# Performance work log

Hardware: AMD Instinct MI355X
Metric: run time of the kernel (lower is better)

## Reference

```python
import jax, jax.numpy as jnp
import numpy as np

B = 131072      # batch size
ORDER = 8       # number of TT modes
N = 64          # grid points per mode (dims[i])
R = 32          # internal TT rank
EPS = 1e-8      # stability_eps
INIT_SCALE = 0.01


def setup_inputs() -> dict:
    key = jax.random.key(0)
    k_idx, k0, kmid, klast = jax.random.split(key, 4)
    indices = jax.random.randint(k_idx, (B, ORDER), 0, N, dtype=jnp.int64)
    # TT cores: core0 (1, N, R), middle cores (ORDER-2, R, N, R), core_last (R, N, 1)
    core0 = jax.random.normal(k0, (1, N, R), dtype=jnp.float32) * INIT_SCALE
    cores_mid = jax.random.normal(kmid, (ORDER - 2, R, N, R), dtype=jnp.float32) * INIT_SCALE
    core_last = jax.random.normal(klast, (R, N, 1), dtype=jnp.float32) * INIT_SCALE
    return {"indices": indices, "core0": core0, "cores_mid": cores_mid, "core_last": core_last}


def _tt_forward(indices, core0, cores_mid, core_last):
    order = 2 + cores_mid.shape[0]
    dims = jnp.array([core0.shape[1]] + [cores_mid.shape[2]] * cores_mid.shape[0]
                     + [core_last.shape[1]], dtype=indices.dtype)
    idx = jnp.clip(indices, 0, dims[None, :] - 1)

    # i == 0: core0[:, idx, :] -> [1, B, R] -> squeeze leading rank-1 -> [B, R]
    v = core0[0, idx[:, 0], :]

    def step(v, core, col_idx):
        sl = core[:, col_idx, :]                                  # [R, B, R']
        norm = jnp.linalg.norm(v, axis=1, keepdims=True) + EPS    # [B, 1]
        v_new = jnp.einsum('br,rbs->bs', v / norm, sl) * norm     # [B, R']
        return v_new

    # middle cores share shape -> scan over them (gather + normalized matvec chain)
    def scan_body(v, inputs):
        core, col = inputs
        return step(v, core, col), None

    mid_cols = idx[:, 1:order - 1].T  # [ORDER-2, B]
    v, _ = jax.lax.scan(scan_body, v, (cores_mid, mid_cols))

    # last core -> [B, 1] -> squeeze -> [B]
    v = step(v, core_last, idx[:, order - 1])
    return v[:, 0]


def reference(indices, core0, cores_mid, core_last):
    return _tt_forward(indices, core0, cores_mid, core_last)
```

## Files before the change

kernel.cpp:

```cpp
#include <hip/hip_runtime.h>
#include <hip/hip_fp16.h>


#define B_TOTAL 131072
#define NDIM 64
#define RANK 32
#define S_BLK 512
#define THREADS 512
#define VSTRIDE_H 40

typedef _Float16 half8  __attribute__((ext_vector_type(8)));
typedef float    f32x4  __attribute__((ext_vector_type(4)));

__global__ __launch_bounds__(256) void build_tables(
    const float* __restrict__ core0, const float* __restrict__ mid,
    const float* __restrict__ lastc,
    half8* __restrict__ PKB, __half* __restrict__ T01, float* __restrict__ TL)
{
    const int id = blockIdx.x * 256 + threadIdx.x;
    if (id < 32768) {
        const int l  = id & 63;
        const int f  = (id >> 6) & 1;
        const int c  = (id >> 7) & 63;
        const int tt = id >> 13;
        const int q = l >> 4, li = l & 15;
        const int n = f * 16 + li;
        const int t = 1 + tt;
        half8 h;
        #pragma unroll
        for (int j = 0; j < 8; ++j) {
            const int k = q * 8 + j;
            h[j] = (_Float16)(16.0f * mid[((t * 32 + k) * 64 + c) * 32 + n]);
        }
        PKB[id] = h;
    } else if (id < 163840) {
        const int i2 = id - 32768;
        const int s = i2 & 31, c1 = (i2 >> 5) & 63, c0 = i2 >> 11;
        float acc = 0.f;
        #pragma unroll
        for (int r = 0; r < 32; ++r)
            acc = fmaf(core0[c0 * 32 + r], mid[(r * 64 + c1) * 32 + s], acc);
        T01[(c0 * 64 + c1) * 32 + s] = __float2half(acc * 256.0f);
    } else {
        const int i3 = id - 163840;
        const int c7 = i3 & 63, c6 = (i3 >> 6) & 63, r = i3 >> 12;
        const float* m5 = mid + 5 * 65536;
        float acc = 0.f;
        #pragma unroll
        for (int s = 0; s < 32; ++s)
            acc = fmaf(m5[(r * 64 + c6) * 32 + s], lastc[s * 64 + c7], acc);
        TL[(c6 * 64 + c7) * 32 + r] = acc * 256.0f;
    }
}

__global__ __launch_bounds__(512) void tt_main_mfma(
    const int* __restrict__ idx, const __half* __restrict__ T01,
    const half8* __restrict__ PKB, const float* __restrict__ TL,
    float* __restrict__ out)
{
    __shared__ __align__(16) __half vbuf[S_BLK * VSTRIDE_H];
    __shared__ unsigned short ord[4][S_BLK];
    __shared__ unsigned char  cols[S_BLK][8];
    __shared__ unsigned int   bases[4][65];
    __shared__ unsigned int   hist[64];

    const int tid  = threadIdx.x;
    const int lane = tid & 63;
    const int wv   = tid >> 6;
    const int li   = lane & 15;
    const int quad = lane >> 4;
    const int b0   = blockIdx.x * S_BLK;

    #pragma unroll
    for (int k = 0; k < S_BLK * 8; k += THREADS) {
        const int lin = k + tid;
        int v = idx[b0 * 8 + lin];
        v = min(max(v, 0), NDIM - 1);
        cols[lin >> 3][lin & 7] = (unsigned char)v;
    }
    __syncthreads();

    for (int tt = 0; tt < 4; ++tt) {
        if (tid < 64) hist[tid] = 0;
        __syncthreads();
        const unsigned int key = cols[tid][2 + tt];
        const unsigned int rank = atomicAdd(&hist[key], 1u);
        __syncthreads();
        if (tid < 64) {
            const unsigned int v = hist[tid];
            unsigned int inc = v;
            #pragma unroll
            for (int d = 1; d < 64; d <<= 1) {
                const unsigned int n = __shfl_up(inc, d);
                if (lane >= d) inc += n;
            }
            bases[tt][tid] = inc - v;
            if (tid == 63) bases[tt][64] = inc;
        }
        __syncthreads();
        ord[tt][bases[tt][key] + rank] = (unsigned short)tid;
        __syncthreads();
    }

    {
        const int g = tid & 7, gid = tid >> 3;
        #pragma unroll
        for (int it = 0; it < S_BLK / 64; ++it) {
            const int s = it * 64 + gid;
            const int c0 = cols[s][0], c1 = cols[s][1];
            const uint2 q = *reinterpret_cast<const uint2*>(
                T01 + (c0 * 64 + c1) * 32 + 4 * g);
            unsigned int* vp = reinterpret_cast<unsigned int*>(vbuf) + s * (VSTRIDE_H / 2);
            vp[2 * g]     = q.x;
            vp[2 * g + 1] = q.y;
        }
    }
    __syncthreads();

    for (int tt = 0; tt < 4; ++tt) {
        for (int c = wv * 8; c < wv * 8 + 8; ++c) {
            const int start = (int)bases[tt][c];
            const int end   = (int)bases[tt][c + 1];
            if (start == end) continue;
            const half8 bf0 = PKB[((tt * 64 + c) * 2 + 0) * 64 + lane];
            const half8 bf1 = PKB[((tt * 64 + c) * 2 + 1) * 64 + lane];

            for (int p = start; p < end; p += 16) {
                const int pos = min(p + li, end - 1);
                const int sm  = (int)ord[tt][pos];
                const half8 A = *reinterpret_cast<const half8*>(
                    reinterpret_cast<const char*>(vbuf) + sm * 80 + quad * 16);
                f32x4 d0 = {0.f, 0.f, 0.f, 0.f}, d1 = {0.f, 0.f, 0.f, 0.f};
                d0 = __builtin_amdgcn_mfma_f32_16x16x32_f16(A, bf0, d0, 0, 0, 0);
                d1 = __builtin_amdgcn_mfma_f32_16x16x32_f16(A, bf1, d1, 0, 0, 0);
                #pragma unroll
                for (int r = 0; r < 4; ++r) {
                    const int mrow = quad * 4 + r;
                    const int s2 = __shfl(sm, mrow);
                    if (p + mrow < end) {
                        vbuf[s2 * VSTRIDE_H + li]      = __float2half(d0[r]);
                        vbuf[s2 * VSTRIDE_H + 16 + li] = __float2half(d1[r]);
                    }
                }
            }
        }
        __syncthreads();
    }

    {
        const int g = tid & 7, gid = tid >> 3;
        #pragma unroll
        for (int it = 0; it < S_BLK / 64; ++it) {
            const int s = it * 64 + gid;
            const int c6 = cols[s][6], c7 = cols[s][7];
            const unsigned int* vp =
                reinterpret_cast<const unsigned int*>(vbuf) + s * (VSTRIDE_H / 2);
            const __half2 v01 = *reinterpret_cast<const __half2*>(&vp[2 * g]);
            const __half2 v23 = *reinterpret_cast<const __half2*>(&vp[2 * g + 1]);
            const float4 L = *reinterpret_cast<const float4*>(
                TL + (c6 * 64 + c7) * 32 + 4 * g);
            float o = 0.f;
            o = fmaf(__low2float(v01),  L.x, o);
            o = fmaf(__high2float(v01), L.y, o);
            o = fmaf(__low2float(v23),  L.z, o);
            o = fmaf(__high2float(v23), L.w, o);
            o += __shfl_xor(o, 1);
            o += __shfl_xor(o, 2);
            o += __shfl_xor(o, 4);
            if (g == 0) out[b0 + s] = o * 2.3283064365386963e-10f;
        }
    }
}

#define PKB_OFF 0u
#define TL_OFF  524288u
#define T01_OFF 1048576u

extern "C" void kernel_launch(void* const* d_in, const int* in_sizes, int n_in,
                              void* d_out, int out_size, void* d_ws, size_t ws_size,
                              hipStream_t stream) {
    const int*   idx   = (const int*)d_in[0];
    const float* core0 = (const float*)d_in[1];
    const float* mid   = (const float*)d_in[2];
    const float* lastc = (const float*)d_in[3];
    float* out = (float*)d_out;

    half8*  PKB = (half8*)((char*)d_ws + PKB_OFF);
    float*  TL  = (float*)((char*)d_ws + TL_OFF);
    __half* T01 = (__half*)((char*)d_ws + T01_OFF);

    hipLaunchKernelGGL(build_tables, dim3(294912 / 256), dim3(256), 0, stream,
                       core0, mid, lastc, PKB, T01, TL);
    hipLaunchKernelGGL(tt_main_mfma, dim3(B_TOTAL / S_BLK), dim3(THREADS), 0, stream,
                       idx, T01, PKB, TL, out);
}
```

Before: 91.10 us.

## Transpose MFMA operands, batch the four counting sorts, prefetch weights, halve block size

The MFMA operands are swapped so the core slice is the A operand and the gathered sample vectors are B. Each lane can then write its sample's 4 output ranks as one contiguous half4, which removes the per-row shuffles and predicated scalar LDS stores. The four per-mode histogram and scan passes are merged into one pass, with each wave scanning one mode, to cut barriers. PKB fragments for the next column are prefetched in registers. Blocks shrink to 256 samples and 256 threads to double the grid, at the cost of fewer samples per column bucket and more padded MFMA work.

Result: faster. 84.21 us (-7.6%).

```diff
diff --git a/kernel.cpp b/kernel.cpp
--- a/kernel.cpp
+++ b/kernel.cpp
@@ -5,12 +5,13 @@
 #define B_TOTAL 131072
 #define NDIM 64
 #define RANK 32
-#define S_BLK 512
-#define THREADS 512
+#define S_BLK 256
+#define THREADS 256
 #define VSTRIDE_H 40
 
-typedef _Float16 half8  __attribute__((ext_vector_type(8)));
-typedef float    f32x4  __attribute__((ext_vector_type(4)));
+typedef _Float16 half8 __attribute__((ext_vector_type(8)));
+typedef _Float16 half4 __attribute__((ext_vector_type(4)));
+typedef float    f32x4 __attribute__((ext_vector_type(4)));
 
 __global__ __launch_bounds__(256) void build_tables(
     const float* __restrict__ core0, const float* __restrict__ mid,
@@ -53,7 +54,7 @@
     }
 }
 
-__global__ __launch_bounds__(512) void tt_main_mfma(
+__global__ __launch_bounds__(256) void tt_main_t(
     const int* __restrict__ idx, const __half* __restrict__ T01,
     const half8* __restrict__ PKB, const float* __restrict__ TL,
     float* __restrict__ out)
@@ -62,7 +63,7 @@
     __shared__ unsigned short ord[4][S_BLK];
     __shared__ unsigned char  cols[S_BLK][8];
     __shared__ unsigned int   bases[4][65];
-    __shared__ unsigned int   hist[64];
+    __shared__ unsigned int   hist[4][64];
 
     const int tid  = threadIdx.x;
     const int lane = tid & 63;
@@ -78,35 +79,38 @@
         v = min(max(v, 0), NDIM - 1);
         cols[lin >> 3][lin & 7] = (unsigned char)v;
     }
-    __syncthreads();
-
+    hist[tid >> 6][tid & 63] = 0;
+    __syncthreads();
+
+    unsigned int key[4], rank[4];
+    #pragma unroll
     for (int tt = 0; tt < 4; ++tt) {
-        if (tid < 64) hist[tid] = 0;
-        __syncthreads();
-        const unsigned int key = cols[tid][2 + tt];
-        const unsigned int rank = atomicAdd(&hist[key], 1u);
-        __syncthreads();
-        if (tid < 64) {
-            const unsigned int v = hist[tid];
-            unsigned int inc = v;
-            #pragma unroll
-            for (int d = 1; d < 64; d <<= 1) {
-                const unsigned int n = __shfl_up(inc, d);
-                if (lane >= d) inc += n;
-            }
-            bases[tt][tid] = inc - v;
-            if (tid == 63) bases[tt][64] = inc;
-        }
-        __syncthreads();
-        ord[tt][bases[tt][key] + rank] = (unsigned short)tid;
-        __syncthreads();
-    }
+        key[tt]  = cols[tid][2 + tt];
+        rank[tt] = atomicAdd(&hist[tt][key[tt]], 1u);
+    }
+    __syncthreads();
+    {
+        const unsigned int v = hist[wv][lane];
+        unsigned int inc = v;
+        #pragma unroll
+        for (int d = 1; d < 64; d <<= 1) {
+            const unsigned int n = __shfl_up(inc, d);
+            if (lane >= d) inc += n;
+        }
+        bases[wv][lane] = inc - v;
+        if (lane == 63) bases[wv][64] = inc;
+    }
+    __syncthreads();
+    #pragma unroll
+    for (int tt = 0; tt < 4; ++tt)
+        ord[tt][bases[tt][key[tt]] + rank[tt]] = (unsigned short)tid;
+    __syncthreads();
 
     {
         const int g = tid & 7, gid = tid >> 3;
         #pragma unroll
-        for (int it = 0; it < S_BLK / 64; ++it) {
-            const int s = it * 64 + gid;
+        for (int it = 0; it < S_BLK / 32; ++it) {
+            const int s = it * 32 + gid;
             const int c0 = cols[s][0], c1 = cols[s][1];
             const uint2 q = *reinterpret_cast<const uint2*>(
                 T01 + (c0 * 64 + c1) * 32 + 4 * g);
@@ -118,31 +122,37 @@
     __syncthreads();
 
     for (int tt = 0; tt < 4; ++tt) {
-        for (int c = wv * 8; c < wv * 8 + 8; ++c) {
+        const int cbase = wv * 16;
+        half8 A0 = PKB[((tt * 64 + cbase) * 2 + 0) * 64 + lane];
+        half8 A1 = PKB[((tt * 64 + cbase) * 2 + 1) * 64 + lane];
+        for (int ci = 0; ci < 16; ++ci) {
+            const int c = cbase + ci;
+            half8 nA0 = A0, nA1 = A1;
+            if (ci < 15) {
+                nA0 = PKB[((tt * 64 + c + 1) * 2 + 0) * 64 + lane];
+                nA1 = PKB[((tt * 64 + c + 1) * 2 + 1) * 64 + lane];
+            }
             const int start = (int)bases[tt][c];
             const int end   = (int)bases[tt][c + 1];
-            if (start == end) continue;
-            const half8 bf0 = PKB[((tt * 64 + c) * 2 + 0) * 64 + lane];
-            const half8 bf1 = PKB[((tt * 64 + c) * 2 + 1) * 64 + lane];
-
             for (int p = start; p < end; p += 16) {
                 const int pos = min(p + li, end - 1);
                 const int sm  = (int)ord[tt][pos];
-                const half8 A = *reinterpret_cast<const half8*>(
+                const half8 Bv = *reinterpret_cast<const half8*>(
                     reinterpret_cast<const char*>(vbuf) + sm * 80 + quad * 16);
                 f32x4 d0 = {0.f, 0.f, 0.f, 0.f}, d1 = {0.f, 0.f, 0.f, 0.f};
-                d0 = __builtin_amdgcn_mfma_f32_16x16x32_f16(A, bf0, d0, 0, 0, 0);
-                d1 = __builtin_amdgcn_mfma_f32_16x16x32_f16(A, bf1, d1, 0, 0, 0);
+                d0 = __builtin_amdgcn_mfma_f32_16x16x32_f16(A0, Bv, d0, 0, 0, 0);
+                d1 = __builtin_amdgcn_mfma_f32_16x16x32_f16(A1, Bv, d1, 0, 0, 0);
+                half4 w0, w1;
                 #pragma unroll
                 for (int r = 0; r < 4; ++r) {
-                    const int mrow = quad * 4 + r;
-                    const int s2 = __shfl(sm, mrow);
-                    if (p + mrow < end) {
-                        vbuf[s2 * VSTRIDE_H + li]      = __float2half(d0[r]);
-                        vbuf[s2 * VSTRIDE_H + 16 + li] = __float2half(d1[r]);
-                    }
+                    w0[r] = (_Float16)d0[r];
+                    w1[r] = (_Float16)d1[r];
                 }
+                char* base = reinterpret_cast<char*>(vbuf) + sm * 80 + quad * 8;
+                *reinterpret_cast<half4*>(base)      = w0;
+                *reinterpret_cast<half4*>(base + 32) = w1;
             }
+            A0 = nA0; A1 = nA1;
         }
         __syncthreads();
     }
@@ -150,8 +160,8 @@
     {
         const int g = tid & 7, gid = tid >> 3;
         #pragma unroll
-        for (int it = 0; it < S_BLK / 64; ++it) {
-            const int s = it * 64 + gid;
+        for (int it = 0; it < S_BLK / 32; ++it) {
+            const int s = it * 32 + gid;
             const int c6 = cols[s][6], c7 = cols[s][7];
             const unsigned int* vp =
                 reinterpret_cast<const unsigned int*>(vbuf) + s * (VSTRIDE_H / 2);
@@ -191,6 +201,6 @@
 
     hipLaunchKernelGGL(build_tables, dim3(294912 / 256), dim3(256), 0, stream,
                        core0, mid, lastc, PKB, T01, TL);
-    hipLaunchKernelGGL(tt_main_mfma, dim3(B_TOTAL / S_BLK), dim3(THREADS), 0, stream,
+    hipLaunchKernelGGL(tt_main_t, dim3(B_TOTAL / S_BLK), dim3(THREADS), 0, stream,
                        idx, T01, PKB, TL, out);
 }
```
